# Kernel optimization log

Hardware: AMD Instinct MI355X
Metric: run time of the kernel (lower is better)

The kernel has to match this reference:

```python
import jax, jax.numpy as jnp
import numpy as np

B, C, H = 16, 256, 128   # batch, channels (in==out, depthwise), spatial
K, S, P = 3, 2, 1        # kernel, stride, padding (the shape-consistent _Transition config)
LEAVES = 4               # levels=2 -> levels**2


def dwconv(x, w, b, stride, pad):
    # depthwise conv: w is [C,1,K,K] (torch OIHW with groups=C)
    out = jax.lax.conv_general_dilated(
        x, w, (stride, stride), [(pad, pad), (pad, pad)],
        dimension_numbers=('NCHW', 'OIHW', 'NCHW'),
        feature_group_count=x.shape[1])
    return out + b[None, :, None, None]


def maxpool(x, k, s, p):
    # matches nn.MaxPool2d (padding acts as -inf for max)
    return jax.lax.reduce_window(
        x, -jnp.inf, jax.lax.max,
        (1, 1, k, k), (1, 1, s, s),
        [(0, 0), (0, 0), (p, p), (p, p)])


def setup_inputs() -> dict:
    key = jax.random.key(0)
    k0, k1, k2, k3 = jax.random.split(key, 4)
    std = (2.0 / (K * K * C)) ** 0.5  # matches the module's normal_(0, sqrt(2/n)) init
    x = jax.random.normal(k0, (B, C, H, H), jnp.float32)
    maxgate = jax.random.normal(k1, (C, 1, K, K), jnp.float32) * std
    pconvs = jax.random.normal(k2, (C, 1, K, K, LEAVES), jnp.float32) * std  # dw=True
    pgates = jax.random.normal(k3, (C, 1, K, K, 3), jnp.float32) * std       # b=False: (leaves+levels)//2 = 3
    mb = jnp.zeros((C,), jnp.float32)
    pbs = jnp.zeros((C, LEAVES), jnp.float32)
    gbs = jnp.zeros((C, 3), jnp.float32)
    return dict(x=x, maxgate=maxgate, mb=mb, pconvs=pconvs, pbs=pbs,
                pgates=pgates, gbs=gbs)


def reference(x, maxgate, mb, pconvs, pbs, pgates, gbs):
    # max branch: maxpool * depthwise gate conv
    out = maxpool(x, K, S, P) * dwconv(x, maxgate, mb, S, P)

    # leaf stage: 2 sigmoid-gated pool pairs (b=False -> gate2 = 1 - gate1)
    # NOTE: code indexes pgates.select(4, c*2) with gbs.select(1, c)
    leaves = []
    for c in range(LEAVES // 2):
        g1 = jax.nn.sigmoid(dwconv(x, pgates[..., 2 * c], gbs[:, c], S, P))
        p1 = dwconv(x, pconvs[..., 2 * c], pbs[:, 2 * c], S, P)
        p2 = dwconv(x, pconvs[..., 2 * c + 1], pbs[:, 2 * c + 1], S, P)
        leaves.append(g1 * p1)
        leaves.append((1.0 - g1) * p2)

    n0 = leaves[0] + leaves[1]
    n1 = leaves[2] + leaves[3]

    # node stage (kernel_size==3 -> no F.pad); b=False reuses pgates[..., leaves//2 + n] = pgates[...,2]
    g = jax.nn.sigmoid(dwconv(n0, pgates[..., LEAVES // 2], gbs[:, 2], 1, P))
    out = out + n0 * g + n1 * (1.0 - g)
    return out
```

## Files before the change

### kernel.cpp

```cpp
#include <hip/hip_runtime.h>
#include <math.h>

#define TB   256
#define HH   128
#define OHW  64
#define TR   16
#define NT   4
#define XR   37
#define XC   136
#define N0C  68

__device__ __forceinline__ float sigmoidf(float z) {
    return 1.0f / (1.0f + __expf(-z));
}

__global__ __launch_bounds__(TB) void fused_densenet_kernel(
    const float* __restrict__ x,
    const float* __restrict__ maxgate,
    const float* __restrict__ mb,
    const float* __restrict__ pconvs,
    const float* __restrict__ pbs,
    const float* __restrict__ pgates,
    const float* __restrict__ gbs,
    float* __restrict__ out)
{
    __shared__ float xs[XR][XC];
    __shared__ float n0s[TR + 2][N0C];

    const int t     = threadIdx.x;
    const int bid   = blockIdx.x;
    const int tile  = bid & (NT - 1);
    const int plane = bid >> 2;
    const int c     = plane & 255;
    const int r0    = tile * TR;

    float wmax[9], wp0[9], wp1[9], wp2[9], wp3[9], wg0[9], wg2[9];
#pragma unroll
    for (int i = 0; i < 9; ++i) {
        wmax[i] = maxgate[c * 9  + i];
        wg0[i]  = pgates [c * 27 + i * 3 + 0];
        wg2[i]  = pgates [c * 27 + i * 3 + 2];
        wp0[i]  = pconvs [c * 36 + i * 4 + 0];
        wp1[i]  = pconvs [c * 36 + i * 4 + 1];
        wp2[i]  = pconvs [c * 36 + i * 4 + 2];
        wp3[i]  = pconvs [c * 36 + i * 4 + 3];
    }
    const float bmax = mb[c];
    const float bp0 = pbs[c * 4 + 0], bp1 = pbs[c * 4 + 1];
    const float bp2 = pbs[c * 4 + 2], bp3 = pbs[c * 4 + 3];
    const float bg0 = gbs[c * 3 + 0];
    const float bg1 = gbs[c * 3 + 1];
    const float bg2 = gbs[c * 3 + 2];

    const float* xplane = x + (size_t)plane * (HH * HH);
    const int ir0 = 2 * r0 - 3;
    for (int s = t; s < XR * 34; s += TB) {
        const int rr = s / 34;
        const int q  = s - rr * 34;
        float4 v = make_float4(0.f, 0.f, 0.f, 0.f);
        const int ir = ir0 + rr;
        if (q >= 1 && q <= 32 && (unsigned)ir < (unsigned)HH) {
            v = *reinterpret_cast<const float4*>(xplane + ir * HH + (q - 1) * 4);
        }
        *reinterpret_cast<float4*>(&xs[rr][q * 4]) = v;
    }
    __syncthreads();

    if (t < 164) {
        int lr, lc;
        if (t < 66)        { lr = 0;  lc = t;       }
        else if (t < 132)  { lr = 17; lc = t - 66;  }
        else { const int i = t - 132; lr = 1 + (i >> 1); lc = (i & 1) ? 65 : 0; }
        const int gr = r0 - 1 + lr;
        const int gc = lc - 1;
        float n0v = 0.f;
        if ((unsigned)gr < (unsigned)OHW && (unsigned)gc < (unsigned)OHW) {
            float ag = 0.f, a0 = 0.f, a1 = 0.f;
#pragma unroll
            for (int dr = 0; dr < 3; ++dr)
#pragma unroll
                for (int dc = 0; dc < 3; ++dc) {
                    const float v = xs[2 * lr + dr][2 * lc + dc + 1];
                    const int i = dr * 3 + dc;
                    ag += v * wg0[i];
                    a0 += v * wp0[i];
                    a1 += v * wp1[i];
                }
            const float sg = sigmoidf(ag + bg0);
            n0v = sg * (a0 + bp0) + (1.f - sg) * (a1 + bp1);
        }
        n0s[lr][lc] = n0v;
    }

    const int lc64 = t & 63;
    const int lrq  = t >> 6;
    float out1[4], n1[4];
#pragma unroll
    for (int k = 0; k < 4; ++k) {
        const int lr = lrq + 4 * k;
        const int gr = r0 + lr;
        const int gc = lc64;

        float w9[9];
#pragma unroll
        for (int dr = 0; dr < 3; ++dr)
#pragma unroll
            for (int dc = 0; dc < 3; ++dc)
                w9[dr * 3 + dc] = xs[2 * lr + dr + 2][2 * lc64 + dc + 3];

        float mp = -INFINITY;
        float amax = 0.f, a0 = 0.f, a1 = 0.f, a2 = 0.f, a3 = 0.f;
        float ag0 = 0.f, ag2 = 0.f;
#pragma unroll
        for (int i = 0; i < 9; ++i) {
            const int dr = i / 3, dc = i % 3;
            const float v = w9[i];
            amax += v * wmax[i];
            a0   += v * wp0[i];
            a1   += v * wp1[i];
            a2   += v * wp2[i];
            a3   += v * wp3[i];
            ag0  += v * wg0[i];
            ag2  += v * wg2[i];
            const bool valid = ((gr > 0) | (dr > 0)) & ((gc > 0) | (dc > 0));
            mp = fmaxf(mp, valid ? v : -INFINITY);
        }
        const float sg0 = sigmoidf(ag0 + bg0);
        n0s[lr + 1][lc64 + 1] = sg0 * (a0 + bp0) + (1.f - sg0) * (a1 + bp1);
        const float sg1 = sigmoidf(ag2 + bg1);
        n1[k]   = sg1 * (a2 + bp2) + (1.f - sg1) * (a3 + bp3);
        out1[k] = mp * (amax + bmax);
    }
    __syncthreads();

    float* oplane = out + (size_t)plane * (OHW * OHW);
#pragma unroll
    for (int k = 0; k < 4; ++k) {
        const int lr = lrq + 4 * k;
        float ag = 0.f;
#pragma unroll
        for (int dr = 0; dr < 3; ++dr)
#pragma unroll
            for (int dc = 0; dc < 3; ++dc)
                ag += n0s[lr + dr][lc64 + dc] * wg2[dr * 3 + dc];
        const float g   = sigmoidf(ag + bg2);
        const float n0c = n0s[lr + 1][lc64 + 1];
        oplane[(r0 + lr) * OHW + lc64] = out1[k] + n0c * g + n1[k] * (1.f - g);
    }
}

extern "C" void kernel_launch(void* const* d_in, const int* in_sizes, int n_in,
                              void* d_out, int out_size, void* d_ws, size_t ws_size,
                              hipStream_t stream) {
    const float* x       = (const float*)d_in[0];
    const float* maxgate = (const float*)d_in[1];
    const float* mb      = (const float*)d_in[2];
    const float* pconvs  = (const float*)d_in[3];
    const float* pbs     = (const float*)d_in[4];
    const float* pgates  = (const float*)d_in[5];
    const float* gbs     = (const float*)d_in[6];
    float* out           = (float*)d_out;

    const int blocks = 16 * 256 * NT;
    fused_densenet_kernel<<<blocks, TB, 0, stream>>>(
        x, maxgate, mb, pconvs, pbs, pgates, gbs, out);
}
```

Measured before the change: 95.37 us.

## Register-tile 2x2 outputs per thread to reuse shared-memory input windows

Each thread now computes a 2x2 block of outputs instead of four rows spaced four apart. It loads one 5x5 input window from shared memory with float4 reads and reuses it across all seven depthwise convolutions and the max-pool. The node-stage gate conv likewise reads a 4x4 n0 window once using float2 loads, and outputs are written as float2. This cuts the number of LDS reads and index arithmetic per output, at the cost of more live accumulator registers (7x4 accumulators plus 63 weights).

Result: slower. 103.4 us (+8.5%).

```diff
diff --git a/kernel.cpp b/kernel.cpp
--- a/kernel.cpp
+++ b/kernel.cpp
@@ -34,16 +34,16 @@
     const int c     = plane & 255;
     const int r0    = tile * TR;
 
-    float wmax[9], wp0[9], wp1[9], wp2[9], wp3[9], wg0[9], wg2[9];
+    float ws[7][9];
 #pragma unroll
     for (int i = 0; i < 9; ++i) {
-        wmax[i] = maxgate[c * 9  + i];
-        wg0[i]  = pgates [c * 27 + i * 3 + 0];
-        wg2[i]  = pgates [c * 27 + i * 3 + 2];
-        wp0[i]  = pconvs [c * 36 + i * 4 + 0];
-        wp1[i]  = pconvs [c * 36 + i * 4 + 1];
-        wp2[i]  = pconvs [c * 36 + i * 4 + 2];
-        wp3[i]  = pconvs [c * 36 + i * 4 + 3];
+        ws[0][i] = maxgate[c * 9  + i];
+        ws[1][i] = pconvs [c * 36 + i * 4 + 0];
+        ws[2][i] = pconvs [c * 36 + i * 4 + 1];
+        ws[3][i] = pconvs [c * 36 + i * 4 + 2];
+        ws[4][i] = pconvs [c * 36 + i * 4 + 3];
+        ws[5][i] = pgates [c * 27 + i * 3 + 0];
+        ws[6][i] = pgates [c * 27 + i * 3 + 2];
     }
     const float bmax = mb[c];
     const float bp0 = pbs[c * 4 + 0], bp1 = pbs[c * 4 + 1];
@@ -56,13 +56,13 @@
     const int ir0 = 2 * r0 - 3;
     for (int s = t; s < XR * 34; s += TB) {
         const int rr = s / 34;
-        const int q  = s - rr * 34;
+        const int qq = s - rr * 34;
         float4 v = make_float4(0.f, 0.f, 0.f, 0.f);
         const int ir = ir0 + rr;
-        if (q >= 1 && q <= 32 && (unsigned)ir < (unsigned)HH) {
-            v = *reinterpret_cast<const float4*>(xplane + ir * HH + (q - 1) * 4);
-        }
-        *reinterpret_cast<float4*>(&xs[rr][q * 4]) = v;
+        if (qq >= 1 && qq <= 32 && (unsigned)ir < (unsigned)HH) {
+            v = *reinterpret_cast<const float4*>(xplane + ir * HH + (qq - 1) * 4);
+        }
+        *reinterpret_cast<float4*>(&xs[rr][qq * 4]) = v;
     }
     __syncthreads();
 
@@ -82,9 +82,9 @@
                 for (int dc = 0; dc < 3; ++dc) {
                     const float v = xs[2 * lr + dr][2 * lc + dc + 1];
                     const int i = dr * 3 + dc;
-                    ag += v * wg0[i];
-                    a0 += v * wp0[i];
-                    a1 += v * wp1[i];
+                    ag += v * ws[5][i];
+                    a0 += v * ws[1][i];
+                    a1 += v * ws[2][i];
                 }
             const float sg = sigmoidf(ag + bg0);
             n0v = sg * (a0 + bp0) + (1.f - sg) * (a1 + bp1);
@@ -92,61 +92,96 @@
         n0s[lr][lc] = n0v;
     }
 
-    const int lc64 = t & 63;
-    const int lrq  = t >> 6;
-    float out1[4], n1[4];
-#pragma unroll
-    for (int k = 0; k < 4; ++k) {
-        const int lr = lrq + 4 * k;
-        const int gr = r0 + lr;
-        const int gc = lc64;
-
-        float w9[9];
-#pragma unroll
-        for (int dr = 0; dr < 3; ++dr)
-#pragma unroll
-            for (int dc = 0; dc < 3; ++dc)
-                w9[dr * 3 + dc] = xs[2 * lr + dr + 2][2 * lc64 + dc + 3];
-
-        float mp = -INFINITY;
-        float amax = 0.f, a0 = 0.f, a1 = 0.f, a2 = 0.f, a3 = 0.f;
-        float ag0 = 0.f, ag2 = 0.f;
-#pragma unroll
-        for (int i = 0; i < 9; ++i) {
-            const int dr = i / 3, dc = i % 3;
-            const float v = w9[i];
-            amax += v * wmax[i];
-            a0   += v * wp0[i];
-            a1   += v * wp1[i];
-            a2   += v * wp2[i];
-            a3   += v * wp3[i];
-            ag0  += v * wg0[i];
-            ag2  += v * wg2[i];
-            const bool valid = ((gr > 0) | (dr > 0)) & ((gc > 0) | (dc > 0));
-            mp = fmaxf(mp, valid ? v : -INFINITY);
-        }
-        const float sg0 = sigmoidf(ag0 + bg0);
-        n0s[lr + 1][lc64 + 1] = sg0 * (a0 + bp0) + (1.f - sg0) * (a1 + bp1);
-        const float sg1 = sigmoidf(ag2 + bg1);
-        n1[k]   = sg1 * (a2 + bp2) + (1.f - sg1) * (a3 + bp3);
-        out1[k] = mp * (amax + bmax);
-    }
+    const int p   = t & 31;
+    const int q   = t >> 5;
+    const int grA = r0 + 2 * q;
+
+    float acc[7][4];
+#pragma unroll
+    for (int ci = 0; ci < 7; ++ci)
+#pragma unroll
+        for (int o = 0; o < 4; ++o) acc[ci][o] = 0.f;
+    float mp0 = -INFINITY, mp1 = -INFINITY, mp2 = -INFINITY, mp3 = -INFINITY;
+
+#pragma unroll
+    for (int rr = 0; rr < 5; ++rr) {
+        const int xr = 4 * q + 2 + rr;
+        const float  v0 = xs[xr][4 * p + 3];
+        const float4 vv = *reinterpret_cast<const float4*>(&xs[xr][4 * p + 4]);
+        const float v1 = vv.x, v2 = vv.y, v3 = vv.z, v4 = vv.w;
+
+        const float v0m = (p == 0) ? -INFINITY : v0;
+        const float h0  = fmaxf(fmaxf(v0m, v1), v2);
+        const float h1  = fmaxf(fmaxf(v2, v3), v4);
+
+        if (rr <= 2) {
+            const float h0a = (rr == 0 && grA == 0) ? -INFINITY : h0;
+            const float h1a = (rr == 0 && grA == 0) ? -INFINITY : h1;
+            mp0 = fmaxf(mp0, h0a);
+            mp1 = fmaxf(mp1, h1a);
+#pragma unroll
+            for (int ci = 0; ci < 7; ++ci) {
+                acc[ci][0] += v0 * ws[ci][3 * rr] + v1 * ws[ci][3 * rr + 1] + v2 * ws[ci][3 * rr + 2];
+                acc[ci][1] += v2 * ws[ci][3 * rr] + v3 * ws[ci][3 * rr + 1] + v4 * ws[ci][3 * rr + 2];
+            }
+        }
+        if (rr >= 2) {
+            const int kr = rr - 2;
+            mp2 = fmaxf(mp2, h0);
+            mp3 = fmaxf(mp3, h1);
+#pragma unroll
+            for (int ci = 0; ci < 7; ++ci) {
+                acc[ci][2] += v0 * ws[ci][3 * kr] + v1 * ws[ci][3 * kr + 1] + v2 * ws[ci][3 * kr + 2];
+                acc[ci][3] += v2 * ws[ci][3 * kr] + v3 * ws[ci][3 * kr + 1] + v4 * ws[ci][3 * kr + 2];
+            }
+        }
+    }
+
+    const float mpv[4] = { mp0, mp1, mp2, mp3 };
+    float out1[4], n1v[4], n0v[4];
+#pragma unroll
+    for (int o = 0; o < 4; ++o) {
+        const float sg0 = sigmoidf(acc[5][o] + bg0);
+        n0v[o] = sg0 * (acc[1][o] + bp0) + (1.f - sg0) * (acc[2][o] + bp1);
+        const float sg1 = sigmoidf(acc[6][o] + bg1);
+        n1v[o]  = sg1 * (acc[3][o] + bp2) + (1.f - sg1) * (acc[4][o] + bp3);
+        out1[o] = mpv[o] * (acc[0][o] + bmax);
+    }
+    n0s[2 * q + 1][2 * p + 1] = n0v[0];
+    n0s[2 * q + 1][2 * p + 2] = n0v[1];
+    n0s[2 * q + 2][2 * p + 1] = n0v[2];
+    n0s[2 * q + 2][2 * p + 2] = n0v[3];
     __syncthreads();
 
+    float n0w[4][4];
+#pragma unroll
+    for (int r = 0; r < 4; ++r) {
+        const float2 a = *reinterpret_cast<const float2*>(&n0s[2 * q + r][2 * p]);
+        const float2 b = *reinterpret_cast<const float2*>(&n0s[2 * q + r][2 * p + 2]);
+        n0w[r][0] = a.x; n0w[r][1] = a.y; n0w[r][2] = b.x; n0w[r][3] = b.y;
+    }
+    float ag[4] = { 0.f, 0.f, 0.f, 0.f };
+#pragma unroll
+    for (int kr = 0; kr < 3; ++kr)
+#pragma unroll
+        for (int kc = 0; kc < 3; ++kc) {
+            const float w = ws[6][kr * 3 + kc];
+            ag[0] += n0w[kr][kc]         * w;
+            ag[1] += n0w[kr][kc + 1]     * w;
+            ag[2] += n0w[kr + 1][kc]     * w;
+            ag[3] += n0w[kr + 1][kc + 1] * w;
+        }
+    const float n0c[4] = { n0w[1][1], n0w[1][2], n0w[2][1], n0w[2][2] };
+
+    float res[4];
+#pragma unroll
+    for (int o = 0; o < 4; ++o) {
+        const float g = sigmoidf(ag[o] + bg2);
+        res[o] = out1[o] + n0c[o] * g + n1v[o] * (1.f - g);
+    }
     float* oplane = out + (size_t)plane * (OHW * OHW);
-#pragma unroll
-    for (int k = 0; k < 4; ++k) {
-        const int lr = lrq + 4 * k;
-        float ag = 0.f;
-#pragma unroll
-        for (int dr = 0; dr < 3; ++dr)
-#pragma unroll
-            for (int dc = 0; dc < 3; ++dc)
-                ag += n0s[lr + dr][lc64 + dc] * wg2[dr * 3 + dc];
-        const float g   = sigmoidf(ag + bg2);
-        const float n0c = n0s[lr + 1][lc64 + 1];
-        oplane[(r0 + lr) * OHW + lc64] = out1[k] + n0c * g + n1[k] * (1.f - g);
-    }
+    *reinterpret_cast<float2*>(&oplane[grA * OHW + 2 * p])       = make_float2(res[0], res[1]);
+    *reinterpret_cast<float2*>(&oplane[(grA + 1) * OHW + 2 * p]) = make_float2(res[2], res[3]);
 }
 
 extern "C" void kernel_launch(void* const* d_in, const int* in_sizes, int n_in,
```

## Drop shared-memory input staging and read stride-2 windows directly from global

Applied to the files above, without the earlier changes.

Removes the shared xs tile and its cooperative load and barrier. Each thread now reads its 3x3 stride-2 window straight from global memory as one float2 plus one scalar per row, and relies on the cache for overlap between neighbouring threads and between tiles. The halo n0 rows are recomputed from global memory as well, and the n0 centre value is kept in registers. This cuts LDS traffic and one barrier, but adds redundant global loads and less coalesced access patterns.

Result: slower. 140.1 us (+46.9%).

```diff
diff --git a/kernel.cpp b/kernel.cpp
--- a/kernel.cpp
+++ b/kernel.cpp
@@ -6,9 +6,8 @@
 #define OHW  64
 #define TR   16
 #define NT   4
-#define XR   37
-#define XC   136
-#define N0C  68
+#define N0R  18
+#define N0C  66
 
 __device__ __forceinline__ float sigmoidf(float z) {
     return 1.0f / (1.0f + __expf(-z));
@@ -24,26 +23,27 @@
     const float* __restrict__ gbs,
     float* __restrict__ out)
 {
-    __shared__ float xs[XR][XC];
-    __shared__ float n0s[TR + 2][N0C];
+    __shared__ float n0s[N0R][N0C];
 
     const int t     = threadIdx.x;
+    const int lane  = t & 63;
+    const int w     = t >> 6;
     const int bid   = blockIdx.x;
     const int tile  = bid & (NT - 1);
     const int plane = bid >> 2;
     const int c     = plane & 255;
     const int r0    = tile * TR;
 
-    float wmax[9], wp0[9], wp1[9], wp2[9], wp3[9], wg0[9], wg2[9];
+    float ws[7][9];
 #pragma unroll
     for (int i = 0; i < 9; ++i) {
-        wmax[i] = maxgate[c * 9  + i];
-        wg0[i]  = pgates [c * 27 + i * 3 + 0];
-        wg2[i]  = pgates [c * 27 + i * 3 + 2];
-        wp0[i]  = pconvs [c * 36 + i * 4 + 0];
-        wp1[i]  = pconvs [c * 36 + i * 4 + 1];
-        wp2[i]  = pconvs [c * 36 + i * 4 + 2];
-        wp3[i]  = pconvs [c * 36 + i * 4 + 3];
+        ws[0][i] = maxgate[c * 9  + i];
+        ws[1][i] = pconvs [c * 36 + i * 4 + 0];
+        ws[2][i] = pconvs [c * 36 + i * 4 + 1];
+        ws[3][i] = pconvs [c * 36 + i * 4 + 2];
+        ws[4][i] = pconvs [c * 36 + i * 4 + 3];
+        ws[5][i] = pgates [c * 27 + i * 3 + 0];
+        ws[6][i] = pgates [c * 27 + i * 3 + 2];
     }
     const float bmax = mb[c];
     const float bp0 = pbs[c * 4 + 0], bp1 = pbs[c * 4 + 1];
@@ -52,100 +52,87 @@
     const float bg1 = gbs[c * 3 + 1];
     const float bg2 = gbs[c * 3 + 2];
 
-    const float* xplane = x + (size_t)plane * (HH * HH);
-    const int ir0 = 2 * r0 - 3;
-    for (int s = t; s < XR * 34; s += TB) {
-        const int rr = s / 34;
-        const int q  = s - rr * 34;
-        float4 v = make_float4(0.f, 0.f, 0.f, 0.f);
-        const int ir = ir0 + rr;
-        if (q >= 1 && q <= 32 && (unsigned)ir < (unsigned)HH) {
-            v = *reinterpret_cast<const float4*>(xplane + ir * HH + (q - 1) * 4);
+    const float* xp = x + (size_t)plane * (HH * HH);
+
+    float out1k[4], n1k[4], n0k[4];
+#pragma unroll
+    for (int k = 0; k < 4; ++k) {
+        const int lr = 4 * k + w;
+        const int gr = r0 + lr;
+        float acc[7];
+#pragma unroll
+        for (int ci = 0; ci < 7; ++ci) acc[ci] = 0.f;
+        float mp = -INFINITY;
+
+#pragma unroll
+        for (int dr = 0; dr < 3; ++dr) {
+            const int ir = 2 * gr - 1 + dr;
+            if (ir >= 0) {
+                const float* rp = xp + ir * HH;
+                float av = 0.f;
+                if (lane > 0) av = rp[2 * lane - 1];
+                const float2 d2 = *reinterpret_cast<const float2*>(&rp[2 * lane]);
+                const float m0 = (lane > 0) ? av : -INFINITY;
+                mp = fmaxf(mp, fmaxf(fmaxf(m0, d2.x), d2.y));
+#pragma unroll
+                for (int ci = 0; ci < 7; ++ci)
+                    acc[ci] += av   * ws[ci][3 * dr]
+                             + d2.x * ws[ci][3 * dr + 1]
+                             + d2.y * ws[ci][3 * dr + 2];
+            }
         }
-        *reinterpret_cast<float4*>(&xs[rr][q * 4]) = v;
+        const float sg0 = sigmoidf(acc[5] + bg0);
+        const float n0v = sg0 * (acc[1] + bp0) + (1.f - sg0) * (acc[2] + bp1);
+        const float sg1 = sigmoidf(acc[6] + bg1);
+        n1k[k]   = sg1 * (acc[3] + bp2) + (1.f - sg1) * (acc[4] + bp3);
+        out1k[k] = mp * (acc[0] + bmax);
+        n0k[k]   = n0v;
+        n0s[lr + 1][lane + 1] = n0v;
+    }
+
+    if (t < 128) {
+        const int gr = (t < 64) ? (r0 - 1) : (r0 + TR);
+        const int cc = t & 63;
+        const int lr = (t < 64) ? 0 : (TR + 1);
+        float n0v = 0.f;
+        if ((unsigned)gr < (unsigned)OHW) {
+            float a1 = 0.f, a2 = 0.f, a5 = 0.f;
+#pragma unroll
+            for (int dr = 0; dr < 3; ++dr) {
+                const int ir = 2 * gr - 1 + dr;
+                if (ir >= 0) {
+                    const float* rp = xp + ir * HH;
+                    float av = 0.f;
+                    if (cc > 0) av = rp[2 * cc - 1];
+                    const float2 d2 = *reinterpret_cast<const float2*>(&rp[2 * cc]);
+                    a1 += av * ws[1][3 * dr] + d2.x * ws[1][3 * dr + 1] + d2.y * ws[1][3 * dr + 2];
+                    a2 += av * ws[2][3 * dr] + d2.x * ws[2][3 * dr + 1] + d2.y * ws[2][3 * dr + 2];
+                    a5 += av * ws[5][3 * dr] + d2.x * ws[5][3 * dr + 1] + d2.y * ws[5][3 * dr + 2];
+                }
+            }
+            const float sg = sigmoidf(a5 + bg0);
+            n0v = sg * (a1 + bp0) + (1.f - sg) * (a2 + bp1);
+        }
+        n0s[lr][cc + 1] = n0v;
+    } else if (t < 128 + 2 * N0R) {
+        const int i = t - 128;
+        n0s[i >> 1][(i & 1) ? (N0C - 1) : 0] = 0.f;
     }
     __syncthreads();
 
-    if (t < 164) {
-        int lr, lc;
-        if (t < 66)        { lr = 0;  lc = t;       }
-        else if (t < 132)  { lr = 17; lc = t - 66;  }
-        else { const int i = t - 132; lr = 1 + (i >> 1); lc = (i & 1) ? 65 : 0; }
-        const int gr = r0 - 1 + lr;
-        const int gc = lc - 1;
-        float n0v = 0.f;
-        if ((unsigned)gr < (unsigned)OHW && (unsigned)gc < (unsigned)OHW) {
-            float ag = 0.f, a0 = 0.f, a1 = 0.f;
-#pragma unroll
-            for (int dr = 0; dr < 3; ++dr)
-#pragma unroll
-                for (int dc = 0; dc < 3; ++dc) {
-                    const float v = xs[2 * lr + dr][2 * lc + dc + 1];
-                    const int i = dr * 3 + dc;
-                    ag += v * wg0[i];
-                    a0 += v * wp0[i];
-                    a1 += v * wp1[i];
-                }
-            const float sg = sigmoidf(ag + bg0);
-            n0v = sg * (a0 + bp0) + (1.f - sg) * (a1 + bp1);
-        }
-        n0s[lr][lc] = n0v;
-    }
-
-    const int lc64 = t & 63;
-    const int lrq  = t >> 6;
-    float out1[4], n1[4];
+    float* op = out + (size_t)plane * (OHW * OHW);
 #pragma unroll
     for (int k = 0; k < 4; ++k) {
-        const int lr = lrq + 4 * k;
-        const int gr = r0 + lr;
-        const int gc = lc64;
-
-        float w9[9];
-#pragma unroll
-        for (int dr = 0; dr < 3; ++dr)
-#pragma unroll
-            for (int dc = 0; dc < 3; ++dc)
-                w9[dr * 3 + dc] = xs[2 * lr + dr + 2][2 * lc64 + dc + 3];
-
-        float mp = -INFINITY;
-        float amax = 0.f, a0 = 0.f, a1 = 0.f, a2 = 0.f, a3 = 0.f;
-        float ag0 = 0.f, ag2 = 0.f;
-#pragma unroll
-        for (int i = 0; i < 9; ++i) {
-            const int dr = i / 3, dc = i % 3;
-            const float v = w9[i];
-            amax += v * wmax[i];
-            a0   += v * wp0[i];
-            a1   += v * wp1[i];
-            a2   += v * wp2[i];
-            a3   += v * wp3[i];
-            ag0  += v * wg0[i];
-            ag2  += v * wg2[i];
-            const bool valid = ((gr > 0) | (dr > 0)) & ((gc > 0) | (dc > 0));
-            mp = fmaxf(mp, valid ? v : -INFINITY);
-        }
-        const float sg0 = sigmoidf(ag0 + bg0);
-        n0s[lr + 1][lc64 + 1] = sg0 * (a0 + bp0) + (1.f - sg0) * (a1 + bp1);
-        const float sg1 = sigmoidf(ag2 + bg1);
-        n1[k]   = sg1 * (a2 + bp2) + (1.f - sg1) * (a3 + bp3);
-        out1[k] = mp * (amax + bmax);
-    }
-    __syncthreads();
-
-    float* oplane = out + (size_t)plane * (OHW * OHW);
-#pragma unroll
-    for (int k = 0; k < 4; ++k) {
-        const int lr = lrq + 4 * k;
+        const int lr = 4 * k + w;
         float ag = 0.f;
 #pragma unroll
-        for (int dr = 0; dr < 3; ++dr)
-#pragma unroll
-            for (int dc = 0; dc < 3; ++dc)
-                ag += n0s[lr + dr][lc64 + dc] * wg2[dr * 3 + dc];
-        const float g   = sigmoidf(ag + bg2);
-        const float n0c = n0s[lr + 1][lc64 + 1];
-        oplane[(r0 + lr) * OHW + lc64] = out1[k] + n0c * g + n1[k] * (1.f - g);
+        for (int dr = 0; dr < 3; ++dr) {
+            ag += n0s[lr + dr][lane]     * ws[6][3 * dr]
+                + n0s[lr + dr][lane + 1] * ws[6][3 * dr + 1]
+                + n0s[lr + dr][lane + 2] * ws[6][3 * dr + 2];
+        }
+        const float g = sigmoidf(ag + bg2);
+        op[(r0 + lr) * OHW + lane] = out1k[k] + n0k[k] * g + n1k[k] * (1.f - g);
     }
 }
 
```

## Double row tile per block to 32 rows with 512 threads, cut halo overhead

Applied to the files above, without the earlier changes.

Each block now covers 32 output rows of a plane with 512 threads instead of 16 rows with 256, halving the block count. This lowers the relative cost of the recomputed halo rows of n0 and the overlapping input rows loaded into shared memory. The kernel also keeps the centre n0 value in a register instead of rereading shared memory, and writes output with nontemporal stores. In exchange the shared-memory footprint per block roughly doubles, which may reduce the number of resident blocks per CU.

Result: faster. 86.89 us (-8.9%).

```diff
diff --git a/kernel.cpp b/kernel.cpp
--- a/kernel.cpp
+++ b/kernel.cpp
@@ -1,13 +1,14 @@
 #include <hip/hip_runtime.h>
 #include <math.h>
 
-#define TB   256
+#define TB   512
 #define HH   128
 #define OHW  64
-#define TR   16
-#define NT   4
-#define XR   37
+#define TR   32
+#define NT   2
+#define XR   69
 #define XC   136
+#define N0R  34
 #define N0C  68
 
 __device__ __forceinline__ float sigmoidf(float z) {
@@ -25,25 +26,25 @@
     float* __restrict__ out)
 {
     __shared__ float xs[XR][XC];
-    __shared__ float n0s[TR + 2][N0C];
+    __shared__ float n0s[N0R][N0C];
 
     const int t     = threadIdx.x;
     const int bid   = blockIdx.x;
     const int tile  = bid & (NT - 1);
-    const int plane = bid >> 2;
+    const int plane = bid >> 1;
     const int c     = plane & 255;
     const int r0    = tile * TR;
 
-    float wmax[9], wp0[9], wp1[9], wp2[9], wp3[9], wg0[9], wg2[9];
+    float ws[7][9];
 #pragma unroll
     for (int i = 0; i < 9; ++i) {
-        wmax[i] = maxgate[c * 9  + i];
-        wg0[i]  = pgates [c * 27 + i * 3 + 0];
-        wg2[i]  = pgates [c * 27 + i * 3 + 2];
-        wp0[i]  = pconvs [c * 36 + i * 4 + 0];
-        wp1[i]  = pconvs [c * 36 + i * 4 + 1];
-        wp2[i]  = pconvs [c * 36 + i * 4 + 2];
-        wp3[i]  = pconvs [c * 36 + i * 4 + 3];
+        ws[0][i] = maxgate[c * 9  + i];
+        ws[1][i] = pconvs [c * 36 + i * 4 + 0];
+        ws[2][i] = pconvs [c * 36 + i * 4 + 1];
+        ws[3][i] = pconvs [c * 36 + i * 4 + 2];
+        ws[4][i] = pconvs [c * 36 + i * 4 + 3];
+        ws[5][i] = pgates [c * 27 + i * 3 + 0];
+        ws[6][i] = pgates [c * 27 + i * 3 + 2];
     }
     const float bmax = mb[c];
     const float bp0 = pbs[c * 4 + 0], bp1 = pbs[c * 4 + 1];
@@ -56,22 +57,22 @@
     const int ir0 = 2 * r0 - 3;
     for (int s = t; s < XR * 34; s += TB) {
         const int rr = s / 34;
-        const int q  = s - rr * 34;
+        const int qq = s - rr * 34;
         float4 v = make_float4(0.f, 0.f, 0.f, 0.f);
         const int ir = ir0 + rr;
-        if (q >= 1 && q <= 32 && (unsigned)ir < (unsigned)HH) {
-            v = *reinterpret_cast<const float4*>(xplane + ir * HH + (q - 1) * 4);
+        if (qq >= 1 && qq <= 32 && (unsigned)ir < (unsigned)HH) {
+            v = *reinterpret_cast<const float4*>(xplane + ir * HH + (qq - 1) * 4);
         }
-        *reinterpret_cast<float4*>(&xs[rr][q * 4]) = v;
+        *reinterpret_cast<float4*>(&xs[rr][qq * 4]) = v;
     }
     __syncthreads();
 
-    if (t < 164) {
-        int lr, lc;
-        if (t < 66)        { lr = 0;  lc = t;       }
-        else if (t < 132)  { lr = 17; lc = t - 66;  }
-        else { const int i = t - 132; lr = 1 + (i >> 1); lc = (i & 1) ? 65 : 0; }
-        const int gr = r0 - 1 + lr;
+    if (t < 196) {
+        int lrr, lc;
+        if (t < 66)        { lrr = 0;        lc = t;       }
+        else if (t < 132)  { lrr = N0R - 1;  lc = t - 66;  }
+        else { const int i = t - 132; lrr = 1 + (i >> 1); lc = (i & 1) ? 65 : 0; }
+        const int gr = r0 - 1 + lrr;
         const int gc = lc - 1;
         float n0v = 0.f;
         if ((unsigned)gr < (unsigned)OHW && (unsigned)gc < (unsigned)OHW) {
@@ -80,24 +81,24 @@
             for (int dr = 0; dr < 3; ++dr)
 #pragma unroll
                 for (int dc = 0; dc < 3; ++dc) {
-                    const float v = xs[2 * lr + dr][2 * lc + dc + 1];
+                    const float v = xs[2 * lrr + dr][2 * lc + dc + 1];
                     const int i = dr * 3 + dc;
-                    ag += v * wg0[i];
-                    a0 += v * wp0[i];
-                    a1 += v * wp1[i];
+                    ag += v * ws[5][i];
+                    a0 += v * ws[1][i];
+                    a1 += v * ws[2][i];
                 }
             const float sg = sigmoidf(ag + bg0);
             n0v = sg * (a0 + bp0) + (1.f - sg) * (a1 + bp1);
         }
-        n0s[lr][lc] = n0v;
+        n0s[lrr][lc] = n0v;
     }
 
     const int lc64 = t & 63;
-    const int lrq  = t >> 6;
-    float out1[4], n1[4];
+    const int wq   = t >> 6;
+    float out1[4], n1[4], n0k[4];
 #pragma unroll
     for (int k = 0; k < 4; ++k) {
-        const int lr = lrq + 4 * k;
+        const int lr = wq + 8 * k;
         const int gr = r0 + lr;
         const int gc = lc64;
 
@@ -115,18 +116,20 @@
         for (int i = 0; i < 9; ++i) {
             const int dr = i / 3, dc = i % 3;
             const float v = w9[i];
-            amax += v * wmax[i];
-            a0   += v * wp0[i];
-            a1   += v * wp1[i];
-            a2   += v * wp2[i];
-            a3   += v * wp3[i];
-            ag0  += v * wg0[i];
-            ag2  += v * wg2[i];
+            amax += v * ws[0][i];
+            a0   += v * ws[1][i];
+            a1   += v * ws[2][i];
+            a2   += v * ws[3][i];
+            a3   += v * ws[4][i];
+            ag0  += v * ws[5][i];
+            ag2  += v * ws[6][i];
             const bool valid = ((gr > 0) | (dr > 0)) & ((gc > 0) | (dc > 0));
             mp = fmaxf(mp, valid ? v : -INFINITY);
         }
         const float sg0 = sigmoidf(ag0 + bg0);
-        n0s[lr + 1][lc64 + 1] = sg0 * (a0 + bp0) + (1.f - sg0) * (a1 + bp1);
+        const float n0v = sg0 * (a0 + bp0) + (1.f - sg0) * (a1 + bp1);
+        n0k[k] = n0v;
+        n0s[lr + 1][lc64 + 1] = n0v;
         const float sg1 = sigmoidf(ag2 + bg1);
         n1[k]   = sg1 * (a2 + bp2) + (1.f - sg1) * (a3 + bp3);
         out1[k] = mp * (amax + bmax);
@@ -136,16 +139,16 @@
     float* oplane = out + (size_t)plane * (OHW * OHW);
 #pragma unroll
     for (int k = 0; k < 4; ++k) {
-        const int lr = lrq + 4 * k;
+        const int lr = wq + 8 * k;
         float ag = 0.f;
 #pragma unroll
         for (int dr = 0; dr < 3; ++dr)
-#pragma unroll
-            for (int dc = 0; dc < 3; ++dc)
-                ag += n0s[lr + dr][lc64 + dc] * wg2[dr * 3 + dc];
-        const float g   = sigmoidf(ag + bg2);
-        const float n0c = n0s[lr + 1][lc64 + 1];
-        oplane[(r0 + lr) * OHW + lc64] = out1[k] + n0c * g + n1[k] * (1.f - g);
+            ag += n0s[lr + dr][lc64]     * ws[6][3 * dr]
+                + n0s[lr + dr][lc64 + 1] * ws[6][3 * dr + 1]
+                + n0s[lr + dr][lc64 + 2] * ws[6][3 * dr + 2];
+        const float g = sigmoidf(ag + bg2);
+        const float r = out1[k] + n0k[k] * g + n1[k] * (1.f - g);
+        __builtin_nontemporal_store(r, &oplane[(r0 + lr) * OHW + lc64]);
     }
 }
 
```
